# Optimization experiments

Hardware: AMD Instinct MI355X
Metric: run time of the kernel (lower is better)

The kernel has to match this reference:

```python
import jax, jax.numpy as jnp
import numpy as np

FEAT = 256
NUM_ATOMS = np.array([2048, 1536, 1024, 2048, 512, 1792, 1280, 2048], dtype=np.int32)
B = len(NUM_ATOMS)
N = int(NUM_ATOMS.sum())          # 12288 total atoms
MAXN = int(NUM_ATOMS.max())       # 2048
# Static segment bookkeeping (num_atoms is structural, not data)
_OFFSETS = np.concatenate([[0], np.cumsum(NUM_ATOMS)[:-1]])
SEG = np.repeat(np.arange(B), NUM_ATOMS)            # [N] graph id per atom
POS = np.arange(N) - _OFFSETS[SEG]                  # [N] position within graph
VALID = np.arange(MAXN)[None, :] < NUM_ATOMS[:, None]  # [B, MAXN] key mask


def setup_inputs() -> dict:
    key = jax.random.key(0)
    k1, k2 = jax.random.split(key)
    s = jax.random.normal(k1, (N, FEAT), jnp.float32)
    # dense: feat_dim -> 3*feat_dim, with bias
    W = jax.random.normal(k2, (FEAT, 3 * FEAT), jnp.float32) / np.float32(np.sqrt(FEAT))
    b = jnp.zeros((3 * FEAT,), jnp.float32)
    num_atoms = jnp.asarray(NUM_ATOMS)
    return {"s": s, "W": W, "b": b, "num_atoms": num_atoms}


def _pad(X):
    # scatter flat [N, FEAT] atoms into padded [B, MAXN, FEAT]
    return jnp.zeros((B, MAXN, FEAT), X.dtype).at[SEG, POS].set(X)


def reference(s, W, b, num_atoms):
    qkv = s @ W + b                          # [N, 3*FEAT]
    Q, K, V = jnp.split(qkv, 3, axis=-1)     # each [N, FEAT]
    Qp, Kp, Vp = _pad(Q), _pad(K), _pad(V)   # [B, MAXN, FEAT]
    scale = np.float32(1.0 / np.sqrt(FEAT))
    scores = jnp.einsum('bqd,bkd->bqk', Qp, Kp) * scale   # [B, MAXN, MAXN]
    scores = jnp.where(VALID[:, None, :], scores, -jnp.inf)  # mask padded keys
    att = jax.nn.softmax(scores, axis=-1)
    out = jnp.einsum('bqk,bkd->bqd', att, Vp)             # [B, MAXN, FEAT]
    return out[SEG, POS]                                   # back to flat [N, FEAT]
```

## Files before the change

### kernel.cpp

```cpp
#include <hip/hip_runtime.h>

typedef __attribute__((ext_vector_type(8))) short short8;
typedef __attribute__((ext_vector_type(4))) short s16x4;
typedef __attribute__((ext_vector_type(4))) float f32x4;

#define MFMA16(a,b,c) __builtin_amdgcn_mfma_f32_16x16x32_bf16((a),(b),(c),0,0,0)

__device__ __forceinline__ ushort f2bf(float f){ union{float f; unsigned u;} v; v.f=f; unsigned r=v.u + 0x7fffu + ((v.u>>16)&1u); return (ushort)(r>>16); }
__device__ __forceinline__ float bf2f(ushort u){ union{unsigned u; float f;} v; v.u = ((unsigned)u)<<16; return v.f; }

__global__ void __launch_bounds__(256) cvt_s_bf16(const float* __restrict__ src,
    ushort* __restrict__ dst)
{
    const int idx = blockIdx.x*256 + threadIdx.x;
    f32x4 v = ((const f32x4*)src)[idx];
    s16x4 o;
    o[0]=(short)f2bf(v[0]); o[1]=(short)f2bf(v[1]);
    o[2]=(short)f2bf(v[2]); o[3]=(short)f2bf(v[3]);
    ((s16x4*)dst)[idx] = o;
}

__global__ void __launch_bounds__(256) transpose_f32_to_bf16(const float* __restrict__ src,
    ushort* __restrict__ dst, int R, int C)
{
    __shared__ __align__(16) ushort tile[64*72];
    const int t = threadIdx.x;
    const int r0 = blockIdx.x*64, c0 = blockIdx.y*64;
    const int rr = t>>2, g = (t&3)*16;
    const float* sp = src + (size_t)(r0+rr)*C + c0 + g;
#pragma unroll
    for (int j=0;j<16;j++) tile[(g+j)*72 + rr] = f2bf(sp[j]);
    __syncthreads();
    ushort* dp = dst + (size_t)(c0+rr)*R + r0 + g;
    *(short8*)dp     = *(const short8*)&tile[rr*72 + g];
    *(short8*)(dp+8) = *(const short8*)&tile[rr*72 + g + 8];
}

__global__ void __launch_bounds__(256) qkv_gemm(const ushort* __restrict__ Sb,
    const ushort* __restrict__ Wt, const float* __restrict__ bias,
    ushort* __restrict__ Q, ushort* __restrict__ K, ushort* __restrict__ Vt)
{
    const int t = threadIdx.x, w = t>>6, l = t&63, lr = l&15, lq = l>>4;
    const int m0 = blockIdx.x*128, n0 = blockIdx.y*64;

    if (n0 < 512){
        f32x4 acc[2][4];
#pragma unroll
        for (int a=0;a<2;a++)
#pragma unroll
            for (int b2=0;b2<4;b2++) acc[a][b2]=(f32x4){0.f,0.f,0.f,0.f};
        const ushort* ap = Sb + (size_t)(m0 + w*32 + lr)*256 + lq*8;
        const ushort* bp = Wt + (size_t)(n0 + lr)*256 + lq*8;
#pragma unroll
        for (int kc=0;kc<8;kc++){
            short8 af0 = *(const short8*)(ap + kc*32);
            short8 af1 = *(const short8*)(ap + 16*256 + kc*32);
#pragma unroll
            for (int nt=0;nt<4;nt++){
                short8 bf = *(const short8*)(bp + (size_t)nt*16*256 + kc*32);
                acc[0][nt] = MFMA16(af0, bf, acc[0][nt]);
                acc[1][nt] = MFMA16(af1, bf, acc[1][nt]);
            }
        }
        ushort* dst = (n0 < 256) ? Q : K;
        const int colbase = n0 & 255;
#pragma unroll
        for (int nt=0;nt<4;nt++){
            float bv = bias[n0 + nt*16 + lr];
#pragma unroll
            for (int mt=0;mt<2;mt++){
                const int row = m0 + w*32 + mt*16 + lq*4;
                ushort* o = dst + (size_t)row*256 + colbase + nt*16 + lr;
#pragma unroll
                for (int i=0;i<4;i++) o[(size_t)i*256] = f2bf(acc[mt][nt][i] + bv);
            }
        }
    } else {
        const int f0 = n0 - 512;
        f32x4 acc[4][2];
#pragma unroll
        for (int a=0;a<4;a++)
#pragma unroll
            for (int b2=0;b2<2;b2++) acc[a][b2]=(f32x4){0.f,0.f,0.f,0.f};
        const ushort* ap = Wt + (size_t)(512 + f0 + lr)*256 + lq*8;
        const ushort* bp = Sb + (size_t)(m0 + w*32 + lr)*256 + lq*8;
#pragma unroll
        for (int kc=0;kc<8;kc++){
            short8 bf0 = *(const short8*)(bp + kc*32);
            short8 bf1 = *(const short8*)(bp + 16*256 + kc*32);
#pragma unroll
            for (int ft=0;ft<4;ft++){
                short8 af = *(const short8*)(ap + (size_t)ft*16*256 + kc*32);
                acc[ft][0] = MFMA16(af, bf0, acc[ft][0]);
                acc[ft][1] = MFMA16(af, bf1, acc[ft][1]);
            }
        }
#pragma unroll
        for (int ft=0;ft<4;ft++){
#pragma unroll
            for (int at=0;at<2;at++){
                ushort* o = Vt + (size_t)(f0 + ft*16 + lq*4)*12288 + m0 + w*32 + at*16 + lr;
#pragma unroll
                for (int i=0;i<4;i++){
                    float bv = bias[512 + f0 + ft*16 + lq*4 + i];
                    o[(size_t)i*12288] = f2bf(acc[ft][at][i] + bv);
                }
            }
        }
    }
}

template<int MODE>
__global__ void __launch_bounds__(256,2) attn_partial(const ushort* __restrict__ Qb,
    const ushort* __restrict__ Kb, const ushort* __restrict__ Vt,
    void* __restrict__ Optr, float* __restrict__ Lptr)
{
    __shared__ __align__(16) ushort Kl[32*264];
    __shared__ __align__(16) ushort Vl[128*40];
    __shared__ __align__(16) ushort Pl[4][32*40];
    const int t = threadIdx.x, w = t>>6, l = t&63, lr = l&15, lq = l>>4;

    const int offs[9]    = {0,2048,3584,4608,6656,7168,8960,10240,12288};
    const int pbase_t[8] = {0,8192,12800,14848,23040,23552,30720,34560};
    const int fh = blockIdx.x & 1, fbase = fh<<7;
    int bi = blockIdx.x >> 1;
    int q0=0, kstart=0, kend=0, off=0, nbg=0, pbase=0;
#pragma unroll
    for (int s=0;s<8;s++){
        const int nb = offs[s+1]-offs[s];
        const int tiles = nb>>7, pieces = (nb+511)>>9;
        const int items = tiles*pieces;
        if (bi >= 0 && bi < items){
            const int tile = bi / pieces, piece = bi - tile*pieces;
            q0 = offs[s] + tile*128;
            kstart = offs[s] + piece*512;
            kend = min(offs[s]+nb, kstart+512);
            off = offs[s]; nbg = nb; pbase = pbase_t[s];
        }
        bi -= items;
    }
    const int nchunks = (kend - kstart) >> 5;
    const int pc = (kstart - off) >> 9;

    short8 qf[2][8];
#pragma unroll
    for (int g=0;g<2;g++){
        const ushort* qp = Qb + (size_t)(q0 + w*32 + g*16 + lr)*256 + lq*8;
#pragma unroll
        for (int kc=0;kc<8;kc++) qf[g][kc] = *(const short8*)(qp + kc*32);
    }
    f32x4 Oa[2][8];
#pragma unroll
    for (int g=0;g<2;g++)
#pragma unroll
        for (int ft=0;ft<8;ft++) Oa[g][ft] = (f32x4){0.f,0.f,0.f,0.f};
    float l_lane[2][4] = {{0.f,0.f,0.f,0.f},{0.f,0.f,0.f,0.f}};

    const int kr = t>>5, kcol = t&31;
    const ushort* kg0 = Kb + (size_t)(kstart + kr)*256 + kcol*8;
    const int vrow = t>>1, vcol = (t&1)*16;
    const ushort* vg0 = Vt + (size_t)(fbase + vrow)*12288 + kstart + vcol;
    short8 kreg[4], vreg[2];
#pragma unroll
    for (int s=0;s<4;s++) kreg[s] = *(const short8*)(kg0 + (size_t)s*8*256);
#pragma unroll
    for (int s=0;s<2;s++) vreg[s] = *(const short8*)(vg0 + s*8);

    for (int ck=0; ck<nchunks; ck++){
#pragma unroll
        for (int s=0;s<4;s++)
            *(short8*)&Kl[(kr + s*8)*264 + kcol*8] = kreg[s];
#pragma unroll
        for (int s=0;s<2;s++)
            *(short8*)&Vl[vrow*40 + vcol + s*8] = vreg[s];
        if (ck+1 < nchunks){
            const ushort* kg = kg0 + (size_t)(ck+1)*32*256;
            const ushort* vg = vg0 + (ck+1)*32;
#pragma unroll
            for (int s=0;s<4;s++) kreg[s] = *(const short8*)(kg + (size_t)s*8*256);
#pragma unroll
            for (int s=0;s<2;s++) vreg[s] = *(const short8*)(vg + s*8);
        }
        __syncthreads();

        f32x4 sc[2][2];
#pragma unroll
        for (int g=0;g<2;g++)
#pragma unroll
            for (int h=0;h<2;h++) sc[g][h] = (f32x4){0.f,0.f,0.f,0.f};
#pragma unroll
        for (int kc=0;kc<8;kc++){
            short8 b0 = *(const short8*)&Kl[ lr     *264 + kc*32 + lq*8];
            short8 b1 = *(const short8*)&Kl[(16+lr)*264 + kc*32 + lq*8];
#pragma unroll
            for (int g=0;g<2;g++){
                sc[g][0] = MFMA16(qf[g][kc], b0, sc[g][0]);
                sc[g][1] = MFMA16(qf[g][kc], b1, sc[g][1]);
            }
        }
        ushort* pw = &Pl[w][0];
#pragma unroll
        for (int g=0;g<2;g++)
#pragma unroll
            for (int i=0;i<4;i++){
                float p0 = exp2f(sc[g][0][i]*0.0901684284f);
                float p1 = exp2f(sc[g][1][i]*0.0901684284f);
                l_lane[g][i] += p0 + p1;
                pw[(g*16+lq*4+i)*40 + lr]      = f2bf(p0);
                pw[(g*16+lq*4+i)*40 + 16 + lr] = f2bf(p1);
            }
        __asm__ volatile("s_waitcnt lgkmcnt(0)" ::: "memory");
        short8 pf0 = *(const short8*)&pw[ lr     *40 + lq*8];
        short8 pf1 = *(const short8*)&pw[(16+lr)*40 + lq*8];

#pragma unroll
        for (int ft=0;ft<8;ft++){
            short8 vf = *(const short8*)&Vl[(ft*16+lr)*40 + lq*8];
            Oa[0][ft] = MFMA16(pf0, vf, Oa[0][ft]);
            Oa[1][ft] = MFMA16(pf1, vf, Oa[1][ft]);
        }
        __syncthreads();
    }

    if (fh == 0){
#pragma unroll
        for (int g=0;g<2;g++)
#pragma unroll
            for (int i=0;i<4;i++){
                float r = l_lane[g][i];
                r += __shfl_xor(r,1); r += __shfl_xor(r,2);
                r += __shfl_xor(r,4); r += __shfl_xor(r,8);
                l_lane[g][i] = r;
            }
    }

    if constexpr (MODE == 0){
        ushort* Op = (ushort*)Optr;
#pragma unroll
        for (int g=0;g<2;g++)
#pragma unroll
            for (int i=0;i<4;i++){
                const int q = q0 + w*32 + g*16 + lq*4 + i;
                ushort* o = Op + (size_t)(pbase + pc*nbg + (q - off))*256 + fbase + lr;
#pragma unroll
                for (int ft=0;ft<8;ft++) o[ft*16] = f2bf(Oa[g][ft][i]);
            }
        if (fh == 0 && lr == 0){
#pragma unroll
            for (int g=0;g<2;g++)
#pragma unroll
                for (int i=0;i<4;i++){
                    const int q = q0 + w*32 + g*16 + lq*4 + i;
                    Lptr[pbase + pc*nbg + (q - off)] = l_lane[g][i];
                }
        }
    } else {
        float* out = (float*)Optr;
#pragma unroll
        for (int g=0;g<2;g++){
            float* op = out + (size_t)(q0 + w*32 + g*16 + lq*4)*256 + fbase + lr;
#pragma unroll
            for (int i=0;i<4;i++)
#pragma unroll
                for (int ft=0;ft<8;ft++)
                    atomicAdd(&op[(size_t)i*256 + ft*16], Oa[g][ft][i]);
        }
        if (fh == 0 && lr == 0){
#pragma unroll
            for (int g=0;g<2;g++)
#pragma unroll
                for (int i=0;i<4;i++)
                    atomicAdd(&Lptr[q0 + w*32 + g*16 + lq*4 + i], l_lane[g][i]);
        }
    }
}

__global__ void __launch_bounds__(256) reduce_norm(const ushort* __restrict__ Opart,
    const float* __restrict__ Lpart, float* __restrict__ out)
{
    const int offs[9]    = {0,2048,3584,4608,6656,7168,8960,10240,12288};
    const int pbase_t[8] = {0,8192,12800,14848,23040,23552,30720,34560};
    const int pieces_t[8]= {4,3,2,4,1,4,3,4};
    const int row = blockIdx.x, t = threadIdx.x;
    int s = 0;
#pragma unroll
    for (int i=0;i<8;i++) if (row >= offs[i+1]) s = i+1;
    const int nb = offs[s+1]-offs[s], S = pieces_t[s];
    const int base = pbase_t[s] + (row - offs[s]);
    float acc = 0.f, L = 0.f;
    for (int p=0; p<S; p++){
        const size_t pr = (size_t)(base + p*nb);
        L   += Lpart[pr];
        acc += bf2f(Opart[pr*256 + t]);
    }
    out[(size_t)row*256 + t] = acc / L;
}

__global__ void __launch_bounds__(256) normalize_out(float* __restrict__ out,
    const float* __restrict__ lsum)
{
    const int row = blockIdx.x, t = threadIdx.x;
    const float inv = 1.0f / lsum[row];
    out[(size_t)row*256 + t] *= inv;
}

extern "C" void kernel_launch(void* const* d_in, const int* in_sizes, int n_in,
                              void* d_out, int out_size, void* d_ws, size_t ws_size,
                              hipStream_t stream)
{
    const float* S    = nullptr;
    const float* W    = nullptr;
    const float* bias = nullptr;
    for (int i = 0; i < n_in; i++){
        if      (in_sizes[i] == 3145728) S    = (const float*)d_in[i];
        else if (in_sizes[i] ==  196608) W    = (const float*)d_in[i];
        else if (in_sizes[i] ==     768) bias = (const float*)d_in[i];
    }
    if (!S)    S    = (const float*)d_in[0];
    if (!W)    W    = (const float*)d_in[1];
    if (!bias) bias = (const float*)d_in[2];

    float* out = (float*)d_out;

    ushort* ws  = (ushort*)d_ws;
    ushort* Wt  = ws;
    ushort* Qb  = Wt + 768*256;
    ushort* Kb  = Qb + 12288*256;
    ushort* Vtb = Kb + 12288*256;

    const size_t base_b  = ((size_t)768*256 + 3*(size_t)12288*256) * 2;
    const size_t opart_b = (size_t)42752*256*2;
    const size_t lpart_b = (size_t)42752*4;
    const bool mode0 = (ws_size >= base_b + opart_b + lpart_b);

    ushort* Sb = (ushort*)d_out;

    cvt_s_bf16           <<<3072,        256, 0, stream>>>(S, Sb);
    transpose_f32_to_bf16<<<dim3(4,12),  256, 0, stream>>>(W, Wt, 256, 768);
    qkv_gemm             <<<dim3(96,12), 256, 0, stream>>>(Sb, Wt, bias, Qb, Kb, Vtb);

    if (mode0){
        ushort* Opart = (ushort*)((char*)d_ws + base_b);
        float*  Lpart = (float*)((char*)d_ws + base_b + opart_b);
        attn_partial<0><<<668, 256, 0, stream>>>(Qb, Kb, Vtb, (void*)Opart, Lpart);
        reduce_norm    <<<12288, 256, 0, stream>>>(Opart, Lpart, out);
    } else {
        float* lsum = (float*)((char*)d_ws + base_b);
        (void)hipMemsetAsync(d_out, 0, (size_t)12288*256*4, stream);
        (void)hipMemsetAsync(lsum,  0, (size_t)12288*4,     stream);
        attn_partial<1><<<668, 256, 0, stream>>>(Qb, Kb, Vtb, (void*)out, lsum);
        normalize_out  <<<12288, 256, 0, stream>>>(out, lsum);
    }
}
```

Baseline: 179.7 us.

## Halve attention query tile, stage W in LDS, vectorize reduce and convert kernels

New measurement: 158.8 us. -11.6%, faster.

```diff
diff --git a/kernel.cpp b/kernel.cpp
--- a/kernel.cpp
+++ b/kernel.cpp
@@ -12,12 +12,16 @@
 __global__ void __launch_bounds__(256) cvt_s_bf16(const float* __restrict__ src,
     ushort* __restrict__ dst)
 {
-    const int idx = blockIdx.x*256 + threadIdx.x;
-    f32x4 v = ((const f32x4*)src)[idx];
-    s16x4 o;
-    o[0]=(short)f2bf(v[0]); o[1]=(short)f2bf(v[1]);
-    o[2]=(short)f2bf(v[2]); o[3]=(short)f2bf(v[3]);
-    ((s16x4*)dst)[idx] = o;
+    const int tid = blockIdx.x*256 + threadIdx.x;
+#pragma unroll
+    for (int r=0;r<3;r++){
+        const int idx = tid + r*262144;
+        f32x4 v = ((const f32x4*)src)[idx];
+        s16x4 o;
+        o[0]=(short)f2bf(v[0]); o[1]=(short)f2bf(v[1]);
+        o[2]=(short)f2bf(v[2]); o[3]=(short)f2bf(v[3]);
+        ((s16x4*)dst)[idx] = o;
+    }
 }
 
 __global__ void __launch_bounds__(256) transpose_f32_to_bf16(const float* __restrict__ src,
@@ -40,9 +44,17 @@
     const ushort* __restrict__ Wt, const float* __restrict__ bias,
     ushort* __restrict__ Q, ushort* __restrict__ K, ushort* __restrict__ Vt)
 {
+    __shared__ __align__(16) ushort Bl[64*264];
     const int t = threadIdx.x, w = t>>6, l = t&63, lr = l&15, lq = l>>4;
     const int m0 = blockIdx.x*128, n0 = blockIdx.y*64;
 
+#pragma unroll
+    for (int s=0;s<8;s++){
+        const int u = t + s*256, row = u>>5, c8 = u&31;
+        *(short8*)&Bl[row*264 + c8*8] = *(const short8*)(Wt + (size_t)(n0+row)*256 + c8*8);
+    }
+    __syncthreads();
+
     if (n0 < 512){
         f32x4 acc[2][4];
 #pragma unroll
@@ -50,14 +62,13 @@
 #pragma unroll
             for (int b2=0;b2<4;b2++) acc[a][b2]=(f32x4){0.f,0.f,0.f,0.f};
         const ushort* ap = Sb + (size_t)(m0 + w*32 + lr)*256 + lq*8;
-        const ushort* bp = Wt + (size_t)(n0 + lr)*256 + lq*8;
 #pragma unroll
         for (int kc=0;kc<8;kc++){
             short8 af0 = *(const short8*)(ap + kc*32);
             short8 af1 = *(const short8*)(ap + 16*256 + kc*32);
 #pragma unroll
             for (int nt=0;nt<4;nt++){
-                short8 bf = *(const short8*)(bp + (size_t)nt*16*256 + kc*32);
+                short8 bf = *(const short8*)&Bl[(nt*16+lr)*264 + lq*8 + kc*32];
                 acc[0][nt] = MFMA16(af0, bf, acc[0][nt]);
                 acc[1][nt] = MFMA16(af1, bf, acc[1][nt]);
             }
@@ -82,7 +93,6 @@
         for (int a=0;a<4;a++)
 #pragma unroll
             for (int b2=0;b2<2;b2++) acc[a][b2]=(f32x4){0.f,0.f,0.f,0.f};
-        const ushort* ap = Wt + (size_t)(512 + f0 + lr)*256 + lq*8;
         const ushort* bp = Sb + (size_t)(m0 + w*32 + lr)*256 + lq*8;
 #pragma unroll
         for (int kc=0;kc<8;kc++){
@@ -90,7 +100,7 @@
             short8 bf1 = *(const short8*)(bp + 16*256 + kc*32);
 #pragma unroll
             for (int ft=0;ft<4;ft++){
-                short8 af = *(const short8*)(ap + (size_t)ft*16*256 + kc*32);
+                short8 af = *(const short8*)&Bl[(ft*16+lr)*264 + lq*8 + kc*32];
                 acc[ft][0] = MFMA16(af, bf0, acc[ft][0]);
                 acc[ft][1] = MFMA16(af, bf1, acc[ft][1]);
             }
@@ -117,7 +127,7 @@
 {
     __shared__ __align__(16) ushort Kl[32*264];
     __shared__ __align__(16) ushort Vl[128*40];
-    __shared__ __align__(16) ushort Pl[4][32*40];
+    __shared__ __align__(16) ushort Pl[4][16*40];
     const int t = threadIdx.x, w = t>>6, l = t&63, lr = l&15, lq = l>>4;
 
     const int offs[9]    = {0,2048,3584,4608,6656,7168,8960,10240,12288};
@@ -128,11 +138,11 @@
 #pragma unroll
     for (int s=0;s<8;s++){
         const int nb = offs[s+1]-offs[s];
-        const int tiles = nb>>7, pieces = (nb+511)>>9;
+        const int tiles = nb>>6, pieces = (nb+511)>>9;
         const int items = tiles*pieces;
         if (bi >= 0 && bi < items){
             const int tile = bi / pieces, piece = bi - tile*pieces;
-            q0 = offs[s] + tile*128;
+            q0 = offs[s] + tile*64;
             kstart = offs[s] + piece*512;
             kend = min(offs[s]+nb, kstart+512);
             off = offs[s]; nbg = nb; pbase = pbase_t[s];
@@ -142,19 +152,16 @@
     const int nchunks = (kend - kstart) >> 5;
     const int pc = (kstart - off) >> 9;
 
-    short8 qf[2][8];
-#pragma unroll
-    for (int g=0;g<2;g++){
-        const ushort* qp = Qb + (size_t)(q0 + w*32 + g*16 + lr)*256 + lq*8;
-#pragma unroll
-        for (int kc=0;kc<8;kc++) qf[g][kc] = *(const short8*)(qp + kc*32);
-    }
-    f32x4 Oa[2][8];
-#pragma unroll
-    for (int g=0;g<2;g++)
-#pragma unroll
-        for (int ft=0;ft<8;ft++) Oa[g][ft] = (f32x4){0.f,0.f,0.f,0.f};
-    float l_lane[2][4] = {{0.f,0.f,0.f,0.f},{0.f,0.f,0.f,0.f}};
+    short8 qf[8];
+    {
+        const ushort* qp = Qb + (size_t)(q0 + w*16 + lr)*256 + lq*8;
+#pragma unroll
+        for (int kc=0;kc<8;kc++) qf[kc] = *(const short8*)(qp + kc*32);
+    }
+    f32x4 Oa[8];
+#pragma unroll
+    for (int ft=0;ft<8;ft++) Oa[ft] = (f32x4){0.f,0.f,0.f,0.f};
+    float l_lane[4] = {0.f,0.f,0.f,0.f};
 
     const int kr = t>>5, kcol = t&31;
     const ushort* kg0 = Kb + (size_t)(kstart + kr)*256 + kcol*8;
@@ -183,94 +190,74 @@
         }
         __syncthreads();
 
-        f32x4 sc[2][2];
-#pragma unroll
-        for (int g=0;g<2;g++)
-#pragma unroll
-            for (int h=0;h<2;h++) sc[g][h] = (f32x4){0.f,0.f,0.f,0.f};
+        f32x4 sc[2];
+        sc[0] = (f32x4){0.f,0.f,0.f,0.f};
+        sc[1] = (f32x4){0.f,0.f,0.f,0.f};
 #pragma unroll
         for (int kc=0;kc<8;kc++){
             short8 b0 = *(const short8*)&Kl[ lr     *264 + kc*32 + lq*8];
             short8 b1 = *(const short8*)&Kl[(16+lr)*264 + kc*32 + lq*8];
-#pragma unroll
-            for (int g=0;g<2;g++){
-                sc[g][0] = MFMA16(qf[g][kc], b0, sc[g][0]);
-                sc[g][1] = MFMA16(qf[g][kc], b1, sc[g][1]);
-            }
+            sc[0] = MFMA16(qf[kc], b0, sc[0]);
+            sc[1] = MFMA16(qf[kc], b1, sc[1]);
         }
         ushort* pw = &Pl[w][0];
 #pragma unroll
-        for (int g=0;g<2;g++)
-#pragma unroll
-            for (int i=0;i<4;i++){
-                float p0 = exp2f(sc[g][0][i]*0.0901684284f);
-                float p1 = exp2f(sc[g][1][i]*0.0901684284f);
-                l_lane[g][i] += p0 + p1;
-                pw[(g*16+lq*4+i)*40 + lr]      = f2bf(p0);
-                pw[(g*16+lq*4+i)*40 + 16 + lr] = f2bf(p1);
-            }
+        for (int i=0;i<4;i++){
+            float p0 = exp2f(sc[0][i]*0.0901684284f);
+            float p1 = exp2f(sc[1][i]*0.0901684284f);
+            l_lane[i] += p0 + p1;
+            pw[(lq*4+i)*40 + lr]      = f2bf(p0);
+            pw[(lq*4+i)*40 + 16 + lr] = f2bf(p1);
+        }
         __asm__ volatile("s_waitcnt lgkmcnt(0)" ::: "memory");
-        short8 pf0 = *(const short8*)&pw[ lr     *40 + lq*8];
-        short8 pf1 = *(const short8*)&pw[(16+lr)*40 + lq*8];
+        short8 pf = *(const short8*)&pw[lr*40 + lq*8];
 
 #pragma unroll
         for (int ft=0;ft<8;ft++){
             short8 vf = *(const short8*)&Vl[(ft*16+lr)*40 + lq*8];
-            Oa[0][ft] = MFMA16(pf0, vf, Oa[0][ft]);
-            Oa[1][ft] = MFMA16(pf1, vf, Oa[1][ft]);
+            Oa[ft] = MFMA16(pf, vf, Oa[ft]);
         }
         __syncthreads();
     }
 
     if (fh == 0){
 #pragma unroll
-        for (int g=0;g<2;g++)
-#pragma unroll
-            for (int i=0;i<4;i++){
-                float r = l_lane[g][i];
-                r += __shfl_xor(r,1); r += __shfl_xor(r,2);
-                r += __shfl_xor(r,4); r += __shfl_xor(r,8);
-                l_lane[g][i] = r;
-            }
+        for (int i=0;i<4;i++){
+            float r = l_lane[i];
+            r += __shfl_xor(r,1); r += __shfl_xor(r,2);
+            r += __shfl_xor(r,4); r += __shfl_xor(r,8);
+            l_lane[i] = r;
+        }
     }
 
     if constexpr (MODE == 0){
         ushort* Op = (ushort*)Optr;
 #pragma unroll
-        for (int g=0;g<2;g++)
+        for (int i=0;i<4;i++){
+            const int q = q0 + w*16 + lq*4 + i;
+            ushort* o = Op + (size_t)(pbase + pc*nbg + (q - off))*256 + fbase + lr;
+#pragma unroll
+            for (int ft=0;ft<8;ft++) o[ft*16] = f2bf(Oa[ft][i]);
+        }
+        if (fh == 0 && lr == 0){
 #pragma unroll
             for (int i=0;i<4;i++){
-                const int q = q0 + w*32 + g*16 + lq*4 + i;
-                ushort* o = Op + (size_t)(pbase + pc*nbg + (q - off))*256 + fbase + lr;
-#pragma unroll
-                for (int ft=0;ft<8;ft++) o[ft*16] = f2bf(Oa[g][ft][i]);
-            }
-        if (fh == 0 && lr == 0){
-#pragma unroll
-            for (int g=0;g<2;g++)
-#pragma unroll
-                for (int i=0;i<4;i++){
-                    const int q = q0 + w*32 + g*16 + lq*4 + i;
-                    Lptr[pbase + pc*nbg + (q - off)] = l_lane[g][i];
-                }
+                const int q = q0 + w*16 + lq*4 + i;
+                Lptr[pbase + pc*nbg + (q - off)] = l_lane[i];
+            }
         }
     } else {
         float* out = (float*)Optr;
-#pragma unroll
-        for (int g=0;g<2;g++){
-            float* op = out + (size_t)(q0 + w*32 + g*16 + lq*4)*256 + fbase + lr;
+        float* op = out + (size_t)(q0 + w*16 + lq*4)*256 + fbase + lr;
+#pragma unroll
+        for (int i=0;i<4;i++)
+#pragma unroll
+            for (int ft=0;ft<8;ft++)
+                atomicAdd(&op[(size_t)i*256 + ft*16], Oa[ft][i]);
+        if (fh == 0 && lr == 0){
 #pragma unroll
             for (int i=0;i<4;i++)
-#pragma unroll
-                for (int ft=0;ft<8;ft++)
-                    atomicAdd(&op[(size_t)i*256 + ft*16], Oa[g][ft][i]);
-        }
-        if (fh == 0 && lr == 0){
-#pragma unroll
-            for (int g=0;g<2;g++)
-#pragma unroll
-                for (int i=0;i<4;i++)
-                    atomicAdd(&Lptr[q0 + w*32 + g*16 + lq*4 + i], l_lane[g][i]);
+                atomicAdd(&Lptr[q0 + w*16 + lq*4 + i], l_lane[i]);
         }
     }
 }
@@ -281,19 +268,30 @@
     const int offs[9]    = {0,2048,3584,4608,6656,7168,8960,10240,12288};
     const int pbase_t[8] = {0,8192,12800,14848,23040,23552,30720,34560};
     const int pieces_t[8]= {4,3,2,4,1,4,3,4};
-    const int row = blockIdx.x, t = threadIdx.x;
+    const int t = threadIdx.x;
+    const int row = blockIdx.x*8 + (t>>5);
+    const int f = (t&31)*8;
     int s = 0;
 #pragma unroll
     for (int i=0;i<8;i++) if (row >= offs[i+1]) s = i+1;
     const int nb = offs[s+1]-offs[s], S = pieces_t[s];
     const int base = pbase_t[s] + (row - offs[s]);
-    float acc = 0.f, L = 0.f;
+    float acc[8] = {0.f,0.f,0.f,0.f,0.f,0.f,0.f,0.f};
+    float L = 0.f;
     for (int p=0; p<S; p++){
         const size_t pr = (size_t)(base + p*nb);
-        L   += Lpart[pr];
-        acc += bf2f(Opart[pr*256 + t]);
-    }
-    out[(size_t)row*256 + t] = acc / L;
+        L += Lpart[pr];
+        short8 v = *(const short8*)&Opart[pr*256 + f];
+#pragma unroll
+        for (int j=0;j<8;j++) acc[j] += bf2f((ushort)v[j]);
+    }
+    const float inv = 1.0f / L;
+    f32x4 o0, o1;
+#pragma unroll
+    for (int j=0;j<4;j++){ o0[j] = acc[j]*inv; o1[j] = acc[4+j]*inv; }
+    float* op = out + (size_t)row*256 + f;
+    *(f32x4*)op     = o0;
+    *(f32x4*)(op+4) = o1;
 }
 
 __global__ void __launch_bounds__(256) normalize_out(float* __restrict__ out,
@@ -335,20 +333,20 @@
 
     ushort* Sb = (ushort*)d_out;
 
-    cvt_s_bf16           <<<3072,        256, 0, stream>>>(S, Sb);
+    cvt_s_bf16           <<<1024,        256, 0, stream>>>(S, Sb);
     transpose_f32_to_bf16<<<dim3(4,12),  256, 0, stream>>>(W, Wt, 256, 768);
     qkv_gemm             <<<dim3(96,12), 256, 0, stream>>>(Sb, Wt, bias, Qb, Kb, Vtb);
 
     if (mode0){
         ushort* Opart = (ushort*)((char*)d_ws + base_b);
         float*  Lpart = (float*)((char*)d_ws + base_b + opart_b);
-        attn_partial<0><<<668, 256, 0, stream>>>(Qb, Kb, Vtb, (void*)Opart, Lpart);
-        reduce_norm    <<<12288, 256, 0, stream>>>(Opart, Lpart, out);
+        attn_partial<0><<<1336, 256, 0, stream>>>(Qb, Kb, Vtb, (void*)Opart, Lpart);
+        reduce_norm    <<<1536, 256, 0, stream>>>(Opart, Lpart, out);
     } else {
         float* lsum = (float*)((char*)d_ws + base_b);
         (void)hipMemsetAsync(d_out, 0, (size_t)12288*256*4, stream);
         (void)hipMemsetAsync(lsum,  0, (size_t)12288*4,     stream);
-        attn_partial<1><<<668, 256, 0, stream>>>(Qb, Kb, Vtb, (void*)out, lsum);
+        attn_partial<1><<<1336, 256, 0, stream>>>(Qb, Kb, Vtb, (void*)out, lsum);
         normalize_out  <<<12288, 256, 0, stream>>>(out, lsum);
     }
 }
```

## Make attention waves independent, stage W in LDS, fuse prep kernels, vectorize reduce

Applied to the files above, without the earlier changes.

After: 251.7 us. 1.4x slower.

```diff
diff --git a/kernel.cpp b/kernel.cpp
--- a/kernel.cpp
+++ b/kernel.cpp
@@ -9,40 +9,51 @@
 __device__ __forceinline__ ushort f2bf(float f){ union{float f; unsigned u;} v; v.f=f; unsigned r=v.u + 0x7fffu + ((v.u>>16)&1u); return (ushort)(r>>16); }
 __device__ __forceinline__ float bf2f(ushort u){ union{unsigned u; float f;} v; v.u = ((unsigned)u)<<16; return v.f; }
 
-__global__ void __launch_bounds__(256) cvt_s_bf16(const float* __restrict__ src,
-    ushort* __restrict__ dst)
-{
-    const int idx = blockIdx.x*256 + threadIdx.x;
-    f32x4 v = ((const f32x4*)src)[idx];
-    s16x4 o;
-    o[0]=(short)f2bf(v[0]); o[1]=(short)f2bf(v[1]);
-    o[2]=(short)f2bf(v[2]); o[3]=(short)f2bf(v[3]);
-    ((s16x4*)dst)[idx] = o;
-}
-
-__global__ void __launch_bounds__(256) transpose_f32_to_bf16(const float* __restrict__ src,
-    ushort* __restrict__ dst, int R, int C)
+__global__ void __launch_bounds__(256) prep(const float* __restrict__ S,
+    ushort* __restrict__ Sb, const float* __restrict__ W, ushort* __restrict__ Wt)
 {
     __shared__ __align__(16) ushort tile[64*72];
     const int t = threadIdx.x;
-    const int r0 = blockIdx.x*64, c0 = blockIdx.y*64;
-    const int rr = t>>2, g = (t&3)*16;
-    const float* sp = src + (size_t)(r0+rr)*C + c0 + g;
-#pragma unroll
-    for (int j=0;j<16;j++) tile[(g+j)*72 + rr] = f2bf(sp[j]);
-    __syncthreads();
-    ushort* dp = dst + (size_t)(c0+rr)*R + r0 + g;
-    *(short8*)dp     = *(const short8*)&tile[rr*72 + g];
-    *(short8*)(dp+8) = *(const short8*)&tile[rr*72 + g + 8];
+    if (blockIdx.x < 1024){
+        const int tid = blockIdx.x*256 + t;
+#pragma unroll
+        for (int r=0;r<3;r++){
+            const int idx = tid + r*262144;
+            f32x4 v = ((const f32x4*)S)[idx];
+            s16x4 o;
+            o[0]=(short)f2bf(v[0]); o[1]=(short)f2bf(v[1]);
+            o[2]=(short)f2bf(v[2]); o[3]=(short)f2bf(v[3]);
+            ((s16x4*)Sb)[idx] = o;
+        }
+    } else {
+        const int i = blockIdx.x - 1024;
+        const int r0 = (i&3)*64, c0 = (i>>2)*64;
+        const int rr = t>>2, g = (t&3)*16;
+        const float* sp = W + (size_t)(r0+rr)*768 + c0 + g;
+#pragma unroll
+        for (int j=0;j<16;j++) tile[(g+j)*72 + rr] = f2bf(sp[j]);
+        __syncthreads();
+        ushort* dp = Wt + (size_t)(c0+rr)*256 + r0 + g;
+        *(short8*)dp     = *(const short8*)&tile[rr*72 + g];
+        *(short8*)(dp+8) = *(const short8*)&tile[rr*72 + g + 8];
+    }
 }
 
 __global__ void __launch_bounds__(256) qkv_gemm(const ushort* __restrict__ Sb,
     const ushort* __restrict__ Wt, const float* __restrict__ bias,
     ushort* __restrict__ Q, ushort* __restrict__ K, ushort* __restrict__ Vt)
 {
+    __shared__ __align__(16) ushort Bl[64*264];
     const int t = threadIdx.x, w = t>>6, l = t&63, lr = l&15, lq = l>>4;
     const int m0 = blockIdx.x*128, n0 = blockIdx.y*64;
 
+#pragma unroll
+    for (int s=0;s<8;s++){
+        const int u = t + s*256, row = u>>5, c8 = u&31;
+        *(short8*)&Bl[row*264 + c8*8] = *(const short8*)(Wt + (size_t)(n0+row)*256 + c8*8);
+    }
+    __syncthreads();
+
     if (n0 < 512){
         f32x4 acc[2][4];
 #pragma unroll
@@ -50,14 +61,13 @@
 #pragma unroll
             for (int b2=0;b2<4;b2++) acc[a][b2]=(f32x4){0.f,0.f,0.f,0.f};
         const ushort* ap = Sb + (size_t)(m0 + w*32 + lr)*256 + lq*8;
-        const ushort* bp = Wt + (size_t)(n0 + lr)*256 + lq*8;
 #pragma unroll
         for (int kc=0;kc<8;kc++){
             short8 af0 = *(const short8*)(ap + kc*32);
             short8 af1 = *(const short8*)(ap + 16*256 + kc*32);
 #pragma unroll
             for (int nt=0;nt<4;nt++){
-                short8 bf = *(const short8*)(bp + (size_t)nt*16*256 + kc*32);
+                short8 bf = *(const short8*)&Bl[(nt*16+lr)*264 + lq*8 + kc*32];
                 acc[0][nt] = MFMA16(af0, bf, acc[0][nt]);
                 acc[1][nt] = MFMA16(af1, bf, acc[1][nt]);
             }
@@ -82,7 +92,6 @@
         for (int a=0;a<4;a++)
 #pragma unroll
             for (int b2=0;b2<2;b2++) acc[a][b2]=(f32x4){0.f,0.f,0.f,0.f};
-        const ushort* ap = Wt + (size_t)(512 + f0 + lr)*256 + lq*8;
         const ushort* bp = Sb + (size_t)(m0 + w*32 + lr)*256 + lq*8;
 #pragma unroll
         for (int kc=0;kc<8;kc++){
@@ -90,7 +99,7 @@
             short8 bf1 = *(const short8*)(bp + 16*256 + kc*32);
 #pragma unroll
             for (int ft=0;ft<4;ft++){
-                short8 af = *(const short8*)(ap + (size_t)ft*16*256 + kc*32);
+                short8 af = *(const short8*)&Bl[(ft*16+lr)*264 + lq*8 + kc*32];
                 acc[ft][0] = MFMA16(af, bf0, acc[ft][0]);
                 acc[ft][1] = MFMA16(af, bf1, acc[ft][1]);
             }
@@ -115,37 +124,36 @@
     const ushort* __restrict__ Kb, const ushort* __restrict__ Vt,
     void* __restrict__ Optr, float* __restrict__ Lptr)
 {
-    __shared__ __align__(16) ushort Kl[32*264];
-    __shared__ __align__(16) ushort Vl[128*40];
     __shared__ __align__(16) ushort Pl[4][32*40];
     const int t = threadIdx.x, w = t>>6, l = t&63, lr = l&15, lq = l>>4;
 
+    const int bid = blockIdx.x;
+    const int item = ((bid & 7)*84 + (bid >> 3))*4 + w;
+    if (item >= 2672) return;
+
     const int offs[9]    = {0,2048,3584,4608,6656,7168,8960,10240,12288};
     const int pbase_t[8] = {0,8192,12800,14848,23040,23552,30720,34560};
-    const int fh = blockIdx.x & 1, fbase = fh<<7;
-    int bi = blockIdx.x >> 1;
-    int q0=0, kstart=0, kend=0, off=0, nbg=0, pbase=0;
-#pragma unroll
-    for (int s=0;s<8;s++){
-        const int nb = offs[s+1]-offs[s];
-        const int tiles = nb>>7, pieces = (nb+511)>>9;
-        const int items = tiles*pieces;
-        if (bi >= 0 && bi < items){
-            const int tile = bi / pieces, piece = bi - tile*pieces;
-            q0 = offs[s] + tile*128;
-            kstart = offs[s] + piece*512;
-            kend = min(offs[s]+nb, kstart+512);
-            off = offs[s]; nbg = nb; pbase = pbase_t[s];
-        }
-        bi -= items;
-    }
+    int rem = item, idx = 0, off = 0, nbg = 0, pbase = 0;
+#pragma unroll
+    for (int i=0;i<8;i++){
+        const int nb = offs[i+1]-offs[i];
+        const int items_g = (nb>>5)*((nb+511)>>9)*2;
+        if (rem >= 0 && rem < items_g){ off=offs[i]; nbg=nb; pbase=pbase_t[i]; idx=rem; }
+        rem -= items_g;
+    }
+    const int tiles = nbg>>5;
+    const int piecefh = idx / tiles, tile = idx - piecefh*tiles;
+    const int fh = piecefh & 1, piece = piecefh >> 1;
+    const int fbase = fh<<7;
+    const int q0 = off + tile*32;
+    const int kstart = off + piece*512;
+    const int kend = min(off + nbg, kstart + 512);
     const int nchunks = (kend - kstart) >> 5;
-    const int pc = (kstart - off) >> 9;
 
     short8 qf[2][8];
 #pragma unroll
     for (int g=0;g<2;g++){
-        const ushort* qp = Qb + (size_t)(q0 + w*32 + g*16 + lr)*256 + lq*8;
+        const ushort* qp = Qb + (size_t)(q0 + g*16 + lr)*256 + lq*8;
 #pragma unroll
         for (int kc=0;kc<8;kc++) qf[g][kc] = *(const short8*)(qp + kc*32);
     }
@@ -156,33 +164,12 @@
         for (int ft=0;ft<8;ft++) Oa[g][ft] = (f32x4){0.f,0.f,0.f,0.f};
     float l_lane[2][4] = {{0.f,0.f,0.f,0.f},{0.f,0.f,0.f,0.f}};
 
-    const int kr = t>>5, kcol = t&31;
-    const ushort* kg0 = Kb + (size_t)(kstart + kr)*256 + kcol*8;
-    const int vrow = t>>1, vcol = (t&1)*16;
-    const ushort* vg0 = Vt + (size_t)(fbase + vrow)*12288 + kstart + vcol;
-    short8 kreg[4], vreg[2];
-#pragma unroll
-    for (int s=0;s<4;s++) kreg[s] = *(const short8*)(kg0 + (size_t)s*8*256);
-#pragma unroll
-    for (int s=0;s<2;s++) vreg[s] = *(const short8*)(vg0 + s*8);
+    const ushort* kp = Kb + (size_t)(kstart + lr)*256 + lq*8;
+    const ushort* vp = Vt + (size_t)(fbase + lr)*12288 + kstart + lq*8;
+    ushort* pw = &Pl[w][0];
 
     for (int ck=0; ck<nchunks; ck++){
-#pragma unroll
-        for (int s=0;s<4;s++)
-            *(short8*)&Kl[(kr + s*8)*264 + kcol*8] = kreg[s];
-#pragma unroll
-        for (int s=0;s<2;s++)
-            *(short8*)&Vl[vrow*40 + vcol + s*8] = vreg[s];
-        if (ck+1 < nchunks){
-            const ushort* kg = kg0 + (size_t)(ck+1)*32*256;
-            const ushort* vg = vg0 + (ck+1)*32;
-#pragma unroll
-            for (int s=0;s<4;s++) kreg[s] = *(const short8*)(kg + (size_t)s*8*256);
-#pragma unroll
-            for (int s=0;s<2;s++) vreg[s] = *(const short8*)(vg + s*8);
-        }
-        __syncthreads();
-
+        const ushort* kcp = kp + (size_t)ck*32*256;
         f32x4 sc[2][2];
 #pragma unroll
         for (int g=0;g<2;g++)
@@ -190,15 +177,14 @@
             for (int h=0;h<2;h++) sc[g][h] = (f32x4){0.f,0.f,0.f,0.f};
 #pragma unroll
         for (int kc=0;kc<8;kc++){
-            short8 b0 = *(const short8*)&Kl[ lr     *264 + kc*32 + lq*8];
-            short8 b1 = *(const short8*)&Kl[(16+lr)*264 + kc*32 + lq*8];
+            short8 b0 = *(const short8*)(kcp + kc*32);
+            short8 b1 = *(const short8*)(kcp + 16*256 + kc*32);
 #pragma unroll
             for (int g=0;g<2;g++){
                 sc[g][0] = MFMA16(qf[g][kc], b0, sc[g][0]);
                 sc[g][1] = MFMA16(qf[g][kc], b1, sc[g][1]);
             }
         }
-        ushort* pw = &Pl[w][0];
 #pragma unroll
         for (int g=0;g<2;g++)
 #pragma unroll
@@ -215,11 +201,10 @@
 
 #pragma unroll
         for (int ft=0;ft<8;ft++){
-            short8 vf = *(const short8*)&Vl[(ft*16+lr)*40 + lq*8];
+            short8 vf = *(const short8*)(vp + (size_t)ft*16*12288 + ck*32);
             Oa[0][ft] = MFMA16(pf0, vf, Oa[0][ft]);
             Oa[1][ft] = MFMA16(pf1, vf, Oa[1][ft]);
         }
-        __syncthreads();
     }
 
     if (fh == 0){
@@ -236,12 +221,12 @@
 
     if constexpr (MODE == 0){
         ushort* Op = (ushort*)Optr;
+        const int prow0 = pbase + piece*nbg + (q0 - off);
 #pragma unroll
         for (int g=0;g<2;g++)
 #pragma unroll
             for (int i=0;i<4;i++){
-                const int q = q0 + w*32 + g*16 + lq*4 + i;
-                ushort* o = Op + (size_t)(pbase + pc*nbg + (q - off))*256 + fbase + lr;
+                ushort* o = Op + (size_t)(prow0 + g*16 + lq*4 + i)*256 + fbase + lr;
 #pragma unroll
                 for (int ft=0;ft<8;ft++) o[ft*16] = f2bf(Oa[g][ft][i]);
             }
@@ -249,16 +234,14 @@
 #pragma unroll
             for (int g=0;g<2;g++)
 #pragma unroll
-                for (int i=0;i<4;i++){
-                    const int q = q0 + w*32 + g*16 + lq*4 + i;
-                    Lptr[pbase + pc*nbg + (q - off)] = l_lane[g][i];
-                }
+                for (int i=0;i<4;i++)
+                    Lptr[prow0 + g*16 + lq*4 + i] = l_lane[g][i];
         }
     } else {
         float* out = (float*)Optr;
 #pragma unroll
         for (int g=0;g<2;g++){
-            float* op = out + (size_t)(q0 + w*32 + g*16 + lq*4)*256 + fbase + lr;
+            float* op = out + (size_t)(q0 + g*16 + lq*4)*256 + fbase + lr;
 #pragma unroll
             for (int i=0;i<4;i++)
 #pragma unroll
@@ -270,7 +253,7 @@
             for (int g=0;g<2;g++)
 #pragma unroll
                 for (int i=0;i<4;i++)
-                    atomicAdd(&Lptr[q0 + w*32 + g*16 + lq*4 + i], l_lane[g][i]);
+                    atomicAdd(&Lptr[q0 + g*16 + lq*4 + i], l_lane[g][i]);
         }
     }
 }
@@ -281,19 +264,30 @@
     const int offs[9]    = {0,2048,3584,4608,6656,7168,8960,10240,12288};
     const int pbase_t[8] = {0,8192,12800,14848,23040,23552,30720,34560};
     const int pieces_t[8]= {4,3,2,4,1,4,3,4};
-    const int row = blockIdx.x, t = threadIdx.x;
+    const int t = threadIdx.x;
+    const int row = blockIdx.x*8 + (t>>5);
+    const int f = (t&31)*8;
     int s = 0;
 #pragma unroll
     for (int i=0;i<8;i++) if (row >= offs[i+1]) s = i+1;
     const int nb = offs[s+1]-offs[s], S = pieces_t[s];
     const int base = pbase_t[s] + (row - offs[s]);
-    float acc = 0.f, L = 0.f;
+    float acc[8] = {0.f,0.f,0.f,0.f,0.f,0.f,0.f,0.f};
+    float L = 0.f;
     for (int p=0; p<S; p++){
         const size_t pr = (size_t)(base + p*nb);
-        L   += Lpart[pr];
-        acc += bf2f(Opart[pr*256 + t]);
-    }
-    out[(size_t)row*256 + t] = acc / L;
+        L += Lpart[pr];
+        short8 v = *(const short8*)&Opart[pr*256 + f];
+#pragma unroll
+        for (int j=0;j<8;j++) acc[j] += bf2f((ushort)v[j]);
+    }
+    const float inv = 1.0f / L;
+    f32x4 o0, o1;
+#pragma unroll
+    for (int j=0;j<4;j++){ o0[j] = acc[j]*inv; o1[j] = acc[4+j]*inv; }
+    float* op = out + (size_t)row*256 + f;
+    *(f32x4*)op     = o0;
+    *(f32x4*)(op+4) = o1;
 }
 
 __global__ void __launch_bounds__(256) normalize_out(float* __restrict__ out,
@@ -335,20 +329,19 @@
 
     ushort* Sb = (ushort*)d_out;
 
-    cvt_s_bf16           <<<3072,        256, 0, stream>>>(S, Sb);
-    transpose_f32_to_bf16<<<dim3(4,12),  256, 0, stream>>>(W, Wt, 256, 768);
-    qkv_gemm             <<<dim3(96,12), 256, 0, stream>>>(Sb, Wt, bias, Qb, Kb, Vtb);
+    prep     <<<1072,        256, 0, stream>>>(S, Sb, W, Wt);
+    qkv_gemm <<<dim3(96,12), 256, 0, stream>>>(Sb, Wt, bias, Qb, Kb, Vtb);
 
     if (mode0){
         ushort* Opart = (ushort*)((char*)d_ws + base_b);
         float*  Lpart = (float*)((char*)d_ws + base_b + opart_b);
-        attn_partial<0><<<668, 256, 0, stream>>>(Qb, Kb, Vtb, (void*)Opart, Lpart);
-        reduce_norm    <<<12288, 256, 0, stream>>>(Opart, Lpart, out);
+        attn_partial<0><<<672, 256, 0, stream>>>(Qb, Kb, Vtb, (void*)Opart, Lpart);
+        reduce_norm    <<<1536, 256, 0, stream>>>(Opart, Lpart, out);
     } else {
         float* lsum = (float*)((char*)d_ws + base_b);
         (void)hipMemsetAsync(d_out, 0, (size_t)12288*256*4, stream);
         (void)hipMemsetAsync(lsum,  0, (size_t)12288*4,     stream);
-        attn_partial<1><<<668, 256, 0, stream>>>(Qb, Kb, Vtb, (void*)out, lsum);
+        attn_partial<1><<<672, 256, 0, stream>>>(Qb, Kb, Vtb, (void*)out, lsum);
         normalize_out  <<<12288, 256, 0, stream>>>(out, lsum);
     }
 }
```
